# Kernel tuning notes

Measured on AMD Instinct MI355X. Metric: run time of the kernel, lower is better.

The kernel has to match this reference:

```python
import jax, jax.numpy as jnp
import numpy as np

N_NODES = 100000
N_EDGES = 1600000
IN_CH = 128
OUT_CH = 64
HID = 2 * OUT_CH  # 128


def _glorot(key, fan_in, fan_out):
    s = np.sqrt(6.0 / (fan_in + fan_out)).astype(np.float32)
    return jax.random.uniform(key, (fan_in, fan_out), jnp.float32, -s, s)


def setup_inputs() -> dict:
    key = jax.random.key(0)
    ks = jax.random.split(key, 8)
    x = jax.random.normal(ks[0], (N_NODES, IN_CH), jnp.float32)
    edge_index = jax.random.randint(ks[1], (2, N_EDGES), 0, N_NODES, jnp.int32)
    return {
        "x": x,
        "edge_index": edge_index,
        "W1": _glorot(ks[2], IN_CH, HID),
        "b1": jnp.zeros((HID,), jnp.float32),
        "W_mu": _glorot(ks[3], HID, OUT_CH),
        "b_mu": jnp.zeros((OUT_CH,), jnp.float32),
        "W_ls": _glorot(ks[4], HID, OUT_CH),
        "b_ls": jnp.zeros((OUT_CH,), jnp.float32),
    }


def _gcn_layer(x, W, b, src, dst, norm, n):
    # transform -> gather -> edge-normalize -> scatter-add -> bias
    h = x @ W                                   # [N, F_out]
    msg = h[src] * norm[:, None]                # [E+N, F_out]
    agg = jax.ops.segment_sum(msg, dst, num_segments=n)
    return agg + b


def reference(x, edge_index, W1, b1, W_mu, b_mu, W_ls, b_ls):
    n = x.shape[0]
    loops = jnp.arange(n, dtype=edge_index.dtype)
    src = jnp.concatenate([edge_index[0], loops])  # self-loops appended
    dst = jnp.concatenate([edge_index[1], loops])
    # symmetric GCN normalization: deg computed at dst (incl. self-loops)
    deg = jax.ops.segment_sum(jnp.ones_like(dst, x.dtype), dst, num_segments=n)
    dinv = jnp.where(deg > 0, jax.lax.rsqrt(jnp.maximum(deg, 1.0)), 0.0)
    norm = dinv[src] * dinv[dst]                # cached=True: reused by all 3 layers

    h = jax.nn.relu(_gcn_layer(x, W1, b1, src, dst, norm, n))
    # dropout in eval mode -> identity
    mu = _gcn_layer(h, W_mu, b_mu, src, dst, norm, n)
    logstd = _gcn_layer(h, W_ls, b_ls, src, dst, norm, n)
    return mu, logstd
```

## Files before the change

kernel.cpp:

```cpp
#include <hip/hip_runtime.h>
#include <hip/hip_fp16.h>


#define NBUCKET 1024
#define NPB 512

typedef _Float16 half8_t __attribute__((ext_vector_type(8)));
typedef float f32x4_t __attribute__((ext_vector_type(4)));

__global__ __launch_bounds__(256) void prep_hist(const int* __restrict__ dst, int E,
                                                 int chunk, int shift,
                                                 int* __restrict__ blk_hist,
                                                 const float* __restrict__ W1,
                                                 const float* __restrict__ Wmu,
                                                 const float* __restrict__ bmu,
                                                 const float* __restrict__ Wls,
                                                 const float* __restrict__ bls,
                                                 __half* __restrict__ Wt1,
                                                 __half* __restrict__ Wt2,
                                                 float* __restrict__ bias2) {
    int b = blockIdx.x;
    if (b >= NPB) {
        int i = (b - NPB) * 256 + threadIdx.x;
        if (i < 16384) {
            int n = i >> 7, k = i & 127;
            Wt1[i] = __float2half_rn(W1[k * 128 + n]);
            float v = (n < 64) ? Wmu[k * 64 + n] : Wls[k * 64 + (n - 64)];
            Wt2[i] = __float2half_rn(v);
        }
        if (i < 64) {
            bias2[i] = bmu[i];
            bias2[64 + i] = bls[i];
        }
        return;
    }
    __shared__ int hist[NBUCKET];
    for (int i = threadIdx.x; i < NBUCKET; i += 256) hist[i] = 0;
    __syncthreads();
    int beg = b * chunk;
    int end = beg + chunk; if (end > E) end = E;
    for (int i = beg + threadIdx.x; i < end; i += 256)
        atomicAdd(&hist[dst[i] >> shift], 1);
    __syncthreads();
    for (int i = threadIdx.x; i < NBUCKET; i += 256)
        blk_hist[(size_t)b * NBUCKET + i] = hist[i];
}

__global__ __launch_bounds__(256) void col_scan(const int* __restrict__ blk_hist,
                                                int* __restrict__ blk_base,
                                                int* __restrict__ bucket_total) {
    __shared__ int sh[256];
    int q = blockIdx.x, t = threadIdx.x;
    int v0 = blk_hist[(size_t)(2 * t) * NBUCKET + q];
    int v1 = blk_hist[(size_t)(2 * t + 1) * NBUCKET + q];
    int s = v0 + v1;
    sh[t] = s;
    __syncthreads();
    for (int off = 1; off < 256; off <<= 1) {
        int x = (t >= off) ? sh[t - off] : 0;
        __syncthreads();
        sh[t] += x;
        __syncthreads();
    }
    int pre = sh[t] - s;
    blk_base[(size_t)(2 * t) * NBUCKET + q] = pre;
    blk_base[(size_t)(2 * t + 1) * NBUCKET + q] = pre + v0;
    if (t == 255) bucket_total[q] = sh[255];
}

__device__ __forceinline__ int partial_base(const int* __restrict__ total, int b,
                                            int* sh ) {
    int t = threadIdx.x;
    int s = 0;
    for (int i = t; i < b; i += 256) s += total[i];
    sh[t] = s;
    __syncthreads();
    for (int off = 128; off >= 1; off >>= 1) {
        if (t < off) sh[t] += sh[t + off];
        __syncthreads();
    }
    int r = sh[0];
    __syncthreads();
    return r;
}

__global__ __launch_bounds__(256) void scatter_pass(const int* __restrict__ src,
                                                    const int* __restrict__ dst, int E,
                                                    int chunk, int shift,
                                                    const int* __restrict__ bucket_total,
                                                    const int* __restrict__ blk_base,
                                                    long long* __restrict__ part) {
    __shared__ int cur[NBUCKET];
    __shared__ int sh[256];
    int b = blockIdx.x, t = threadIdx.x;
    {
        int idx0 = t * 4;
        int v[4];
#pragma unroll
        for (int k = 0; k < 4; ++k) v[k] = bucket_total[idx0 + k];
        int s = v[0] + v[1] + v[2] + v[3];
        sh[t] = s;
        __syncthreads();
        for (int off = 1; off < 256; off <<= 1) {
            int x = (t >= off) ? sh[t - off] : 0;
            __syncthreads();
            sh[t] += x;
            __syncthreads();
        }
        int run = sh[t] - s;
#pragma unroll
        for (int k = 0; k < 4; ++k) {
            cur[idx0 + k] = run;
            run += v[k];
        }
    }
    __syncthreads();
    for (int i = t; i < NBUCKET; i += 256)
        cur[i] += blk_base[(size_t)b * NBUCKET + i];
    __syncthreads();
    int beg = b * chunk;
    int end = beg + chunk; if (end > E) end = E;
    for (int i = beg + t; i < end; i += 256) {
        int d = dst[i], s = src[i];
        int q = d >> shift;
        int p = atomicAdd(&cur[q], 1);
        part[p] = ((long long)(unsigned)d << 32) | (unsigned)s;
    }
}

__global__ __launch_bounds__(256) void bucket_count(const long long* __restrict__ part,
                                                    const int* __restrict__ bucket_total,
                                                    int N, int shift,
                                                    int* __restrict__ degi,
                                                    float* __restrict__ dinv,
                                                    int* __restrict__ padded_total) {
    __shared__ int cnt[128];
    __shared__ int sh[256];
    int b = blockIdx.x, t = threadIdx.x;
    int beg = partial_base(bucket_total, b, sh);
    int end = beg + bucket_total[b];
    if (t < 128) cnt[t] = 0;
    __syncthreads();
    int node0 = b << shift;
    for (int i = beg + t; i < end; i += 256) {
        int d = (int)((unsigned long long)part[i] >> 32);
        atomicAdd(&cnt[d - node0], 1);
    }
    __syncthreads();
    if (t < 128) {
        int node = node0 + t;
        int c = (node < N) ? cnt[t] : 0;
        if (node < N) {
            degi[node] = c;
            dinv[node] = rsqrtf((float)(c + 1));
        }
        sh[t] = c;
    }
    __syncthreads();
    int padded = 0;
    if (t < 128) {
        int node = node0 + t;
        if (node < N) {
            int mine = (sh[t] + 15) >> 4;
            int pi = t ^ 1;
            int pnode = node0 + pi;
            int theirs = (pnode < N) ? ((sh[pi] + 15) >> 4) : 0;
            int L = mine > theirs ? mine : theirs;
            padded = L << 4;
        }
    }
    __syncthreads();
    if (t < 128) sh[t] = padded; else if (t < 256) sh[t] = 0;
    __syncthreads();
    for (int off = 64; off >= 1; off >>= 1) {
        if (t < off) sh[t] += sh[t + off];
        __syncthreads();
    }
    if (t == 0) padded_total[b] = sh[0];
}

__global__ __launch_bounds__(256) void bucket_fill(const long long* __restrict__ part,
                                                   const int* __restrict__ bucket_total,
                                                   const int* __restrict__ padded_total,
                                                   const int* __restrict__ degi,
                                                   const float* __restrict__ dinv,
                                                   int N, int shift,
                                                   int* __restrict__ row_ptr,
                                                   long long* __restrict__ csr2) {
    __shared__ int sh[256];
    __shared__ int pexcl[128];
    __shared__ int padarr[128];
    __shared__ int cur[128];
    __shared__ float dvl[128];
    int b = blockIdx.x, t = threadIdx.x;
    int node0 = b << shift;
    int ebeg = partial_base(bucket_total, b, sh);
    int eend = ebeg + bucket_total[b];
    int pbase = partial_base(padded_total, b, sh);

    if (t < 128) {
        int node = node0 + t;
        int deg = (node < N) ? degi[node] : 0;
        dvl[t] = (node < N) ? dinv[node] : 0.0f;
        sh[t] = deg;
    }
    __syncthreads();
    int padded = 0;
    if (t < 128) {
        int node = node0 + t;
        if (node < N) {
            int mine = (sh[t] + 15) >> 4;
            int pi = t ^ 1;
            int pnode = node0 + pi;
            int theirs = (pnode < N) ? ((sh[pi] + 15) >> 4) : 0;
            int L = mine > theirs ? mine : theirs;
            padded = L << 4;
        }
        padarr[t] = padded;
    }
    __syncthreads();
    if (t < 128) sh[t] = padded;
    __syncthreads();
    for (int off = 1; off < 128; off <<= 1) {
        int x = 0;
        if (t < 128 && t >= off) x = sh[t - off];
        __syncthreads();
        if (t < 128) sh[t] += x;
        __syncthreads();
    }
    if (t < 128) {
        int excl = sh[t] - padarr[t];
        pexcl[t] = excl;
        cur[t] = pbase + excl;
        int node = node0 + t;
        if (node < N) row_ptr[node] = pbase + excl;
    }
    __syncthreads();
    if (t == 0) {
        int boundary = node0 + 128;
        if (boundary > N) boundary = N;
        row_ptr[boundary] = pbase + sh[127];
    }
    for (int i = ebeg + t; i < eend; i += 256) {
        long long pr = part[i];
        int d = (int)((unsigned long long)pr >> 32);
        int s = (int)(unsigned)(pr & 0xffffffffLL);
        int dl = d - node0;
        int p = atomicAdd(&cur[dl], 1);
        float w = dinv[s] * dvl[dl];
        csr2[p] = (long long)(unsigned)s |
                  ((long long)(unsigned)__float_as_uint(w) << 32);
    }
    __syncthreads();
    if (t < 128) {
        int node = node0 + t;
        if (node < N) {
            int endp = pbase + pexcl[t] + padarr[t];
            long long rec = (long long)(unsigned)node;
            for (int p = cur[t]; p < endp; ++p) csr2[p] = rec;
        }
    }
}

template <int AF32>
__global__ __launch_bounds__(256) void gemm_mfma(const void* __restrict__ Av, int M,
                                                 const __half* __restrict__ Bt,
                                                 __half* __restrict__ C) {
    __shared__ __half Bs[128][136];
    int tid = threadIdx.x;
#pragma unroll
    for (int i = 0; i < 8; ++i) {
        int idx = tid + i * 256;
        int r = idx >> 4;
        int c8 = (idx & 15) << 3;
        *(float4*)&Bs[r][c8] = *(const float4*)(Bt + r * 128 + c8);
    }
    __syncthreads();
    int wave = tid >> 6, lane = tid & 63;
    int lr = lane & 15, lk = lane >> 4;
    int row0 = blockIdx.x * 128 + wave * 32;

    f32x4_t acc[2][8];
#pragma unroll
    for (int rt = 0; rt < 2; ++rt)
#pragma unroll
        for (int ct = 0; ct < 8; ++ct) acc[rt][ct] = (f32x4_t)0.0f;

    half8_t afr[2][4];
#pragma unroll
    for (int rt = 0; rt < 2; ++rt) {
        int row = row0 + rt * 16 + lr;
        if (row >= M) row = M - 1;
        if (AF32) {
            const float* A = (const float*)Av + (size_t)row * 128;
#pragma unroll
            for (int ks = 0; ks < 4; ++ks) {
                float4 v0 = *(const float4*)(A + ks * 32 + lk * 8);
                float4 v1 = *(const float4*)(A + ks * 32 + lk * 8 + 4);
                half8_t f;
                f[0] = (_Float16)v0.x; f[1] = (_Float16)v0.y;
                f[2] = (_Float16)v0.z; f[3] = (_Float16)v0.w;
                f[4] = (_Float16)v1.x; f[5] = (_Float16)v1.y;
                f[6] = (_Float16)v1.z; f[7] = (_Float16)v1.w;
                afr[rt][ks] = f;
            }
        } else {
            const __half* A = (const __half*)Av + (size_t)row * 128;
#pragma unroll
            for (int ks = 0; ks < 4; ++ks)
                afr[rt][ks] = *(const half8_t*)(A + ks * 32 + lk * 8);
        }
    }
#pragma unroll
    for (int ks = 0; ks < 4; ++ks)
#pragma unroll
        for (int ct = 0; ct < 8; ++ct) {
            half8_t b = *(const half8_t*)&Bs[ct * 16 + lr][ks * 32 + lk * 8];
            acc[0][ct] = __builtin_amdgcn_mfma_f32_16x16x32_f16(afr[0][ks], b, acc[0][ct], 0, 0, 0);
            acc[1][ct] = __builtin_amdgcn_mfma_f32_16x16x32_f16(afr[1][ks], b, acc[1][ct], 0, 0, 0);
        }
#pragma unroll
    for (int rt = 0; rt < 2; ++rt)
#pragma unroll
        for (int r = 0; r < 4; ++r) {
            int row = row0 + rt * 16 + lk * 4 + r;
            if (row < M) {
#pragma unroll
                for (int ct = 0; ct < 8; ++ct)
                    C[(size_t)row * 128 + ct * 16 + lr] = __float2half_rn(acc[rt][ct][r]);
            }
        }
}

template <int MODE>
__global__ __launch_bounds__(256) void gather_pair(const __half* __restrict__ h,
                                                   const float* __restrict__ dinv,
                                                   const int* __restrict__ row_ptr,
                                                   const long long* __restrict__ csr2,
                                                   const float* __restrict__ bias,
                                                   void* __restrict__ outv, int n) {
    int wv = (blockIdx.x * 256 + threadIdx.x) >> 6;
    int lane = threadIdx.x & 63;
    int nodeA = wv * 2;
    if (nodeA >= n) return;
    int half = lane >> 5;
    int grp2 = (lane >> 4) & 1;
    int cs = lane & 15;
    int bvalid = (nodeA + 1) < n;
    int wid = nodeA + (half & bvalid);
    float dv = dinv[wid];
    int beg = row_ptr[wid];
    int end = row_ptr[wid + 1];

    float acc[8];
    {
        float4 raw = *(const float4*)(h + (size_t)wid * 128 + cs * 8);
        const __half2* hp = (const __half2*)&raw;
        float sw = (grp2 == 0) ? dv * dv : 0.0f;
#pragma unroll
        for (int q = 0; q < 4; ++q) {
            float2 f = __half22float2(hp[q]);
            acc[2 * q]     = sw * f.x;
            acc[2 * q + 1] = sw * f.y;
        }
    }

    long long e[8];
    if (beg < end) {
#pragma unroll
        for (int u = 0; u < 8; ++u) e[u] = csr2[beg + u * 2 + grp2];
    }
#pragma unroll 1
    for (int j = beg; j < end; j += 16) {
        int jn = j + 16;
        int jp = (jn < end) ? jn : beg;
        long long en[8];
#pragma unroll
        for (int u = 0; u < 8; ++u) en[u] = csr2[jp + u * 2 + grp2];
        float4 raw[8];
        float wgt[8];
#pragma unroll
        for (int u = 0; u < 8; ++u) {
            int s = (int)(unsigned)(e[u] & 0xffffffffLL);
            wgt[u] = __uint_as_float((unsigned)((unsigned long long)e[u] >> 32));
            raw[u] = *(const float4*)(h + (size_t)s * 128 + cs * 8);
        }
#pragma unroll
        for (int u = 0; u < 8; ++u) {
            const __half2* hp = (const __half2*)&raw[u];
#pragma unroll
            for (int q = 0; q < 4; ++q) {
                float2 f = __half22float2(hp[q]);
                acc[2 * q]     = fmaf(wgt[u], f.x, acc[2 * q]);
                acc[2 * q + 1] = fmaf(wgt[u], f.y, acc[2 * q + 1]);
            }
        }
#pragma unroll
        for (int u = 0; u < 8; ++u) e[u] = en[u];
    }

#pragma unroll
    for (int q = 0; q < 8; ++q) acc[q] += __shfl_xor(acc[q], 16, 64);

    {
        const float4* bp = (const float4*)(bias + cs * 8);
        float4 b0 = bp[0], b1 = bp[1];
        if (MODE == 0) {
            acc[0] = fmaxf(acc[0] + b0.x, 0.0f);
            acc[1] = fmaxf(acc[1] + b0.y, 0.0f);
            acc[2] = fmaxf(acc[2] + b0.z, 0.0f);
            acc[3] = fmaxf(acc[3] + b0.w, 0.0f);
            acc[4] = fmaxf(acc[4] + b1.x, 0.0f);
            acc[5] = fmaxf(acc[5] + b1.y, 0.0f);
            acc[6] = fmaxf(acc[6] + b1.z, 0.0f);
            acc[7] = fmaxf(acc[7] + b1.w, 0.0f);
        } else {
            acc[0] += b0.x; acc[1] += b0.y; acc[2] += b0.z; acc[3] += b0.w;
            acc[4] += b1.x; acc[5] += b1.y; acc[6] += b1.z; acc[7] += b1.w;
        }
    }

    if ((lane & 31) < 16 && (half == 0 || bvalid)) {
        if (MODE == 0) {
            union { __half2 h2[4]; float4 f4; } u;
            u.h2[0] = __floats2half2_rn(acc[0], acc[1]);
            u.h2[1] = __floats2half2_rn(acc[2], acc[3]);
            u.h2[2] = __floats2half2_rn(acc[4], acc[5]);
            u.h2[3] = __floats2half2_rn(acc[6], acc[7]);
            *(float4*)((__half*)outv + (size_t)wid * 128 + cs * 8) = u.f4;
        } else {
            float* mu = (float*)outv;
            float* ls = mu + (size_t)n * 64;
            float* op = (cs < 8) ? (mu + (size_t)wid * 64 + cs * 8)
                                 : (ls + (size_t)wid * 64 + (cs - 8) * 8);
            ((float4*)op)[0] = make_float4(acc[0], acc[1], acc[2], acc[3]);
            ((float4*)op)[1] = make_float4(acc[4], acc[5], acc[6], acc[7]);
        }
    }
}

extern "C" void kernel_launch(void* const* d_in, const int* in_sizes, int n_in,
                              void* d_out, int out_size, void* d_ws, size_t ws_size,
                              hipStream_t stream) {
    const float* x   = (const float*)d_in[0];
    const int*  eidx = (const int*)d_in[1];
    const float* W1  = (const float*)d_in[2];
    const float* b1  = (const float*)d_in[3];
    const float* Wmu = (const float*)d_in[4];
    const float* bmu = (const float*)d_in[5];
    const float* Wls = (const float*)d_in[6];
    const float* bls = (const float*)d_in[7];
    float* out = (float*)d_out;

    const int N = in_sizes[0] / 128;
    const int E = in_sizes[1] / 2;
    const int* src = eidx;
    const int* dst = eidx + E;

    int shift = 0;
    while (((N - 1) >> shift) >= NBUCKET) ++shift;
    int chunk = (E + NPB - 1) / NPB;

    char* w = (char*)d_ws;
    size_t off = 0;
    auto alloc = [&](size_t bytes) {
        void* p = w + off;
        off += (bytes + 255) & ~(size_t)255;
        return p;
    };
    int*       row_ptr      = (int*)alloc((size_t)(N + 1) * 4);
    float*     dinv         = (float*)alloc((size_t)N * 4);
    int*       bucket_total = (int*)alloc(NBUCKET * 4);
    int*       padded_total = (int*)alloc(NBUCKET * 4);
    __half*    Wt1          = (__half*)alloc(16384 * 2);
    __half*    Wt2          = (__half*)alloc(16384 * 2);
    float*     bias2        = (float*)alloc(128 * 4);
    size_t csr_cap = (size_t)E + 31u * (size_t)N + 64;
    long long* csr2         = (long long*)alloc(csr_cap * 8);
    __half*    h1           = (__half*)alloc((size_t)N * 128 * 2);
    size_t Dstart = off;
    int*       degi     = (int*)alloc((size_t)N * 4);
    int*       blk_hist = (int*)alloc((size_t)NPB * NBUCKET * 4);
    int*       blk_base = (int*)alloc((size_t)NPB * NBUCKET * 4);
    long long* part     = (long long*)alloc((size_t)E * 8);
    size_t Dearly_end = off;
    __half* h = (__half*)(w + Dstart);
    __half* p = (__half*)(w + Dstart);
    size_t Dend = Dstart + (size_t)N * 128 * 2;
    off = (Dearly_end > Dend) ? Dearly_end : Dend;
    if (off > ws_size) return;

    prep_hist<<<NPB + 64, 256, 0, stream>>>(dst, E, chunk, shift, blk_hist,
                                            W1, Wmu, bmu, Wls, bls, Wt1, Wt2, bias2);
    col_scan<<<NBUCKET, 256, 0, stream>>>(blk_hist, blk_base, bucket_total);
    scatter_pass<<<NPB, 256, 0, stream>>>(src, dst, E, chunk, shift,
                                          bucket_total, blk_base, part);
    bucket_count<<<NBUCKET, 256, 0, stream>>>(part, bucket_total, N, shift,
                                              degi, dinv, padded_total);
    bucket_fill<<<NBUCKET, 256, 0, stream>>>(part, bucket_total, padded_total,
                                             degi, dinv, N, shift, row_ptr, csr2);

    int gemm_blocks = (N + 127) / 128;
    int gblocks = (((N + 1) / 2) * 64 + 255) / 256;
    gemm_mfma<1><<<gemm_blocks, 256, 0, stream>>>(x, N, Wt1, h);
    gather_pair<0><<<gblocks, 256, 0, stream>>>(h, dinv, row_ptr, csr2, b1, h1, N);
    gemm_mfma<0><<<gemm_blocks, 256, 0, stream>>>(h1, N, Wt2, p);
    gather_pair<1><<<gblocks, 256, 0, stream>>>(p, dinv, row_ptr, csr2, bias2, out, N);
}
```

Before: 236.3 us.

## Fold self-loop into CSR and switch gather to one node per wavefront

Each node's self-loop edge with weight dinv^2 now goes directly into the padded CSR. Per-node padding is computed on its own instead of matching the larger of a node pair. The gather kernel now handles one node per wavefront with four 16-lane groups, each reading 4 edges per step, and drops the cross-iteration prefetch of edge records. This cuts padding waste and the separate self-term load, but loses the software prefetch and adds an extra shuffle reduction.

```diff
diff --git a/kernel.cpp b/kernel.cpp
--- a/kernel.cpp
+++ b/kernel.cpp
@@ -147,30 +147,18 @@
         atomicAdd(&cnt[d - node0], 1);
     }
     __syncthreads();
+    int padded = 0;
     if (t < 128) {
         int node = node0 + t;
         int c = (node < N) ? cnt[t] : 0;
         if (node < N) {
             degi[node] = c;
             dinv[node] = rsqrtf((float)(c + 1));
-        }
-        sh[t] = c;
-    }
-    __syncthreads();
-    int padded = 0;
-    if (t < 128) {
-        int node = node0 + t;
-        if (node < N) {
-            int mine = (sh[t] + 15) >> 4;
-            int pi = t ^ 1;
-            int pnode = node0 + pi;
-            int theirs = (pnode < N) ? ((sh[pi] + 15) >> 4) : 0;
-            int L = mine > theirs ? mine : theirs;
-            padded = L << 4;
-        }
-    }
-    __syncthreads();
-    if (t < 128) sh[t] = padded; else if (t < 256) sh[t] = 0;
+            padded = ((c + 16) >> 4) << 4;
+        }
+    }
+    __syncthreads();
+    if (t < 128) sh[t] = padded; else sh[t] = 0;
     __syncthreads();
     for (int off = 64; off >= 1; off >>= 1) {
         if (t < off) sh[t] += sh[t + off];
@@ -198,24 +186,12 @@
     int eend = ebeg + bucket_total[b];
     int pbase = partial_base(padded_total, b, sh);
 
+    int padded = 0;
     if (t < 128) {
         int node = node0 + t;
         int deg = (node < N) ? degi[node] : 0;
         dvl[t] = (node < N) ? dinv[node] : 0.0f;
-        sh[t] = deg;
-    }
-    __syncthreads();
-    int padded = 0;
-    if (t < 128) {
-        int node = node0 + t;
-        if (node < N) {
-            int mine = (sh[t] + 15) >> 4;
-            int pi = t ^ 1;
-            int pnode = node0 + pi;
-            int theirs = (pnode < N) ? ((sh[pi] + 15) >> 4) : 0;
-            int L = mine > theirs ? mine : theirs;
-            padded = L << 4;
-        }
+        if (node < N) padded = ((deg + 16) >> 4) << 4;
         padarr[t] = padded;
     }
     __syncthreads();
@@ -231,9 +207,16 @@
     if (t < 128) {
         int excl = sh[t] - padarr[t];
         pexcl[t] = excl;
-        cur[t] = pbase + excl;
         int node = node0 + t;
-        if (node < N) row_ptr[node] = pbase + excl;
+        if (node < N) {
+            row_ptr[node] = pbase + excl;
+            float ws = dvl[t] * dvl[t];
+            csr2[pbase + excl] = (long long)(unsigned)node |
+                                 ((long long)(unsigned)__float_as_uint(ws) << 32);
+            cur[t] = pbase + excl + 1;
+        } else {
+            cur[t] = pbase + excl;
+        }
     }
     __syncthreads();
     if (t == 0) {
@@ -333,60 +316,35 @@
 }
 
 template <int MODE>
-__global__ __launch_bounds__(256) void gather_pair(const __half* __restrict__ h,
-                                                   const float* __restrict__ dinv,
-                                                   const int* __restrict__ row_ptr,
-                                                   const long long* __restrict__ csr2,
-                                                   const float* __restrict__ bias,
-                                                   void* __restrict__ outv, int n) {
-    int wv = (blockIdx.x * 256 + threadIdx.x) >> 6;
+__global__ __launch_bounds__(256) void gather_one(const __half* __restrict__ h,
+                                                  const int* __restrict__ row_ptr,
+                                                  const long long* __restrict__ csr2,
+                                                  const float* __restrict__ bias,
+                                                  void* __restrict__ outv, int n) {
+    int wid = (blockIdx.x * 256 + threadIdx.x) >> 6;
     int lane = threadIdx.x & 63;
-    int nodeA = wv * 2;
-    if (nodeA >= n) return;
-    int half = lane >> 5;
-    int grp2 = (lane >> 4) & 1;
-    int cs = lane & 15;
-    int bvalid = (nodeA + 1) < n;
-    int wid = nodeA + (half & bvalid);
-    float dv = dinv[wid];
+    if (wid >= n) return;
+    int grp = lane >> 4;
+    int cs  = lane & 15;
     int beg = row_ptr[wid];
     int end = row_ptr[wid + 1];
 
-    float acc[8];
-    {
-        float4 raw = *(const float4*)(h + (size_t)wid * 128 + cs * 8);
-        const __half2* hp = (const __half2*)&raw;
-        float sw = (grp2 == 0) ? dv * dv : 0.0f;
-#pragma unroll
-        for (int q = 0; q < 4; ++q) {
-            float2 f = __half22float2(hp[q]);
-            acc[2 * q]     = sw * f.x;
-            acc[2 * q + 1] = sw * f.y;
-        }
-    }
-
-    long long e[8];
-    if (beg < end) {
-#pragma unroll
-        for (int u = 0; u < 8; ++u) e[u] = csr2[beg + u * 2 + grp2];
-    }
+    float acc[8] = {};
 #pragma unroll 1
     for (int j = beg; j < end; j += 16) {
-        int jn = j + 16;
-        int jp = (jn < end) ? jn : beg;
-        long long en[8];
-#pragma unroll
-        for (int u = 0; u < 8; ++u) en[u] = csr2[jp + u * 2 + grp2];
-        float4 raw[8];
-        float wgt[8];
-#pragma unroll
-        for (int u = 0; u < 8; ++u) {
+        long long e[4];
+#pragma unroll
+        for (int u = 0; u < 4; ++u) e[u] = csr2[j + u * 4 + grp];
+        float4 raw[4];
+        float wgt[4];
+#pragma unroll
+        for (int u = 0; u < 4; ++u) {
             int s = (int)(unsigned)(e[u] & 0xffffffffLL);
             wgt[u] = __uint_as_float((unsigned)((unsigned long long)e[u] >> 32));
             raw[u] = *(const float4*)(h + (size_t)s * 128 + cs * 8);
         }
 #pragma unroll
-        for (int u = 0; u < 8; ++u) {
+        for (int u = 0; u < 4; ++u) {
             const __half2* hp = (const __half2*)&raw[u];
 #pragma unroll
             for (int q = 0; q < 4; ++q) {
@@ -395,12 +353,13 @@
                 acc[2 * q + 1] = fmaf(wgt[u], f.y, acc[2 * q + 1]);
             }
         }
-#pragma unroll
-        for (int u = 0; u < 8; ++u) e[u] = en[u];
-    }
-
-#pragma unroll
-    for (int q = 0; q < 8; ++q) acc[q] += __shfl_xor(acc[q], 16, 64);
+    }
+
+#pragma unroll
+    for (int q = 0; q < 8; ++q) {
+        acc[q] += __shfl_xor(acc[q], 16, 64);
+        acc[q] += __shfl_xor(acc[q], 32, 64);
+    }
 
     {
         const float4* bp = (const float4*)(bias + cs * 8);
@@ -420,7 +379,7 @@
         }
     }
 
-    if ((lane & 31) < 16 && (half == 0 || bvalid)) {
+    if (lane < 16) {
         if (MODE == 0) {
             union { __half2 h2[4]; float4 f4; } u;
             u.h2[0] = __floats2half2_rn(acc[0], acc[1]);
@@ -475,7 +434,7 @@
     __half*    Wt1          = (__half*)alloc(16384 * 2);
     __half*    Wt2          = (__half*)alloc(16384 * 2);
     float*     bias2        = (float*)alloc(128 * 4);
-    size_t csr_cap = (size_t)E + 31u * (size_t)N + 64;
+    size_t csr_cap = (size_t)E + 17u * (size_t)N + 64;
     long long* csr2         = (long long*)alloc(csr_cap * 8);
     __half*    h1           = (__half*)alloc((size_t)N * 128 * 2);
     size_t Dstart = off;
@@ -501,9 +460,9 @@
                                              degi, dinv, N, shift, row_ptr, csr2);
 
     int gemm_blocks = (N + 127) / 128;
-    int gblocks = (((N + 1) / 2) * 64 + 255) / 256;
+    int gblocks = ((size_t)N * 64 + 255) / 256;
     gemm_mfma<1><<<gemm_blocks, 256, 0, stream>>>(x, N, Wt1, h);
-    gather_pair<0><<<gblocks, 256, 0, stream>>>(h, dinv, row_ptr, csr2, b1, h1, N);
+    gather_one<0><<<gblocks, 256, 0, stream>>>(h, row_ptr, csr2, b1, h1, N);
     gemm_mfma<0><<<gemm_blocks, 256, 0, stream>>>(h1, N, Wt2, p);
-    gather_pair<1><<<gblocks, 256, 0, stream>>>(p, dinv, row_ptr, csr2, bias2, out, N);
-}
+    gather_one<1><<<gblocks, 256, 0, stream>>>(p, row_ptr, csr2, bias2, out, N);
+}
```

New measurement: 227.7 us. 1.04x faster.
